# Optimization experiments

Measured on AMD Instinct MI355X. Metric: run time of the kernel, lower is better.

## Reference

```python
import jax, jax.numpy as jnp
import numpy as np

N_CONTEXT = 9
N_INPUT = 26
WINDOW = 2 * N_CONTEXT + 1  # 19
BATCH, TIME = 64, 2000


def setup_inputs() -> dict:
    key = jax.random.key(0)
    x = jax.random.normal(key, (BATCH, TIME, N_INPUT), dtype=jnp.float32)
    return {"x": x}


def reference(x):
    # The original uses conv1d with an identity filter of shape
    # (window, channels, window*channels) and SAME padding. That is exactly
    # a zero-padded sliding-window unfold: output[b, t] = flatten of
    # x[b, t-n_context : t+n_context+1, :] (zero padded at edges).
    B, T, C = x.shape
    xp = jnp.pad(x, ((0, 0), (N_CONTEXT, N_CONTEXT), (0, 0)))  # [B, T+2*ctx, C]
    # gather indices for each output position: [T, WINDOW]
    idx = jnp.arange(T)[:, None] + jnp.arange(WINDOW)[None, :]
    win = xp[:, idx, :]  # [B, T, WINDOW, C]
    return win.reshape(-1, WINDOW * C)  # [B*T, WINDOW*C]
```

## Files before the change

kernel.cpp:

```cpp
#include <hip/hip_runtime.h>

constexpr int N_CONTEXT = 9;
constexpr int C         = 26;
constexpr int WINDOW    = 2 * N_CONTEXT + 1;
constexpr int BATCH     = 64;
constexpr int TIME      = 2000;
constexpr int ROW       = WINDOW * C;

constexpr int T_TILE      = 16;
constexpr int LDS_ROWS    = T_TILE + WINDOW - 1;
constexpr int LDS_FLOATS  = LDS_ROWS * C;
constexpr int TILE_FLOATS = T_TILE * ROW;
constexpr int TILE_VEC4   = TILE_FLOATS / 4;
constexpr int BLOCK       = 256;
constexpr int NBLOCKS     = BATCH * TIME / T_TILE;
constexpr int BATCH_FLOATS = TIME * C;

typedef float vfloat4 __attribute__((ext_vector_type(4)));

__global__ __launch_bounds__(BLOCK)
void CreateOverlappingWindows_84963043050043_kernel(const float* __restrict__ x,
                                                    float* __restrict__ out) {
    __shared__ float lds[LDS_FLOATS];
    const int blk = blockIdx.x;
    const int tid = threadIdx.x;
    const int r0  = blk * T_TILE;
    const int b   = r0 / TIME;
    const int lo  = b * BATCH_FLOATS;
    const int g0  = (r0 - N_CONTEXT) * C;

    #pragma unroll
    for (int it = 0; it < (LDS_FLOATS + BLOCK - 1) / BLOCK; ++it) {
        int idx = tid + it * BLOCK;
        if (idx < LDS_FLOATS) {
            int g = g0 + idx;
            lds[idx] = ((unsigned)(g - lo) < (unsigned)BATCH_FLOATS) ? x[g] : 0.0f;
        }
    }
    __syncthreads();

    const float2* lds2 = reinterpret_cast<const float2*>(lds);
    vfloat4* out4 = reinterpret_cast<vfloat4*>(out) + (size_t)blk * TILE_VEC4;
    #pragma unroll
    for (int it = 0; it < (TILE_VEC4 + BLOCK - 1) / BLOCK; ++it) {
        int q = tid + it * BLOCK;
        if (q < TILE_VEC4) {
            int f  = q * 4;
            int lt = f / ROW;
            int j  = f - lt * ROW;
            int a  = lt * C + j;
            int sub = (j == ROW - 2) ? (ROW - C) : 0;
            float2 p0 = lds2[a >> 1];
            float2 p1 = lds2[(a + 2 - sub) >> 1];
            vfloat4 v; v.x = p0.x; v.y = p0.y; v.z = p1.x; v.w = p1.y;
            out4[q] = v;
        }
    }
}

extern "C" void kernel_launch(void* const* d_in, const int* in_sizes, int n_in,
                              void* d_out, int out_size, void* d_ws, size_t ws_size,
                              hipStream_t stream) {
    const float* x = (const float*)d_in[0];
    float* out = (float*)d_out;
    CreateOverlappingWindows_84963043050043_kernel<<<NBLOCKS, BLOCK, 0, stream>>>(x, out);
}
```

Measured before the change: 252.8 us.

## Enlarge time tile and write output as per-column float2 streams

Raises the tile from 16 to 40 timesteps so the halo overhead per block shrinks, and loads the input into LDS as float2. The output phase now gives each of 247 threads one float2 column and loops over the 40 rows, replacing the earlier flat float4 write with its per-element index math. In exchange, stores are 8-byte rather than 16-byte, 9 of 256 threads sit idle during writes, and a block has 40 dependent store iterations, which may lower memory-level parallelism on a write-bound kernel.

```diff
diff --git a/kernel.cpp b/kernel.cpp
--- a/kernel.cpp
+++ b/kernel.cpp
@@ -6,54 +6,45 @@
 constexpr int BATCH     = 64;
 constexpr int TIME      = 2000;
 constexpr int ROW       = WINDOW * C;
+constexpr int ROW2      = ROW / 2;
+constexpr int C2        = C / 2;
 
-constexpr int T_TILE      = 16;
-constexpr int LDS_ROWS    = T_TILE + WINDOW - 1;
-constexpr int LDS_FLOATS  = LDS_ROWS * C;
-constexpr int TILE_FLOATS = T_TILE * ROW;
-constexpr int TILE_VEC4   = TILE_FLOATS / 4;
-constexpr int BLOCK       = 256;
-constexpr int NBLOCKS     = BATCH * TIME / T_TILE;
-constexpr int BATCH_FLOATS = TIME * C;
-
-typedef float vfloat4 __attribute__((ext_vector_type(4)));
+constexpr int T_TILE    = 40;
+constexpr int LDS_ROWS  = T_TILE + WINDOW - 1;
+constexpr int LDS_F2    = LDS_ROWS * C2;
+constexpr int BLOCK     = 256;
+constexpr int NBLOCKS   = BATCH * TIME / T_TILE;
+constexpr int BATCH_F2  = TIME * C2;
 
 __global__ __launch_bounds__(BLOCK)
 void CreateOverlappingWindows_84963043050043_kernel(const float* __restrict__ x,
                                                     float* __restrict__ out) {
-    __shared__ float lds[LDS_FLOATS];
+    __shared__ float2 lds2[LDS_F2];
     const int blk = blockIdx.x;
     const int tid = threadIdx.x;
     const int r0  = blk * T_TILE;
     const int b   = r0 / TIME;
-    const int lo  = b * BATCH_FLOATS;
-    const int g0  = (r0 - N_CONTEXT) * C;
+    const int lo2 = b * BATCH_F2;
+    const int base2 = ((r0 - N_CONTEXT) * C) >> 1;
+    const float2* x2 = reinterpret_cast<const float2*>(x);
 
     #pragma unroll
-    for (int it = 0; it < (LDS_FLOATS + BLOCK - 1) / BLOCK; ++it) {
+    for (int it = 0; it < (LDS_F2 + BLOCK - 1) / BLOCK; ++it) {
         int idx = tid + it * BLOCK;
-        if (idx < LDS_FLOATS) {
-            int g = g0 + idx;
-            lds[idx] = ((unsigned)(g - lo) < (unsigned)BATCH_FLOATS) ? x[g] : 0.0f;
+        if (idx < LDS_F2) {
+            int g = base2 + idx;
+            float2 v = make_float2(0.0f, 0.0f);
+            if ((unsigned)(g - lo2) < (unsigned)BATCH_F2) v = x2[g];
+            lds2[idx] = v;
         }
     }
     __syncthreads();
 
-    const float2* lds2 = reinterpret_cast<const float2*>(lds);
-    vfloat4* out4 = reinterpret_cast<vfloat4*>(out) + (size_t)blk * TILE_VEC4;
-    #pragma unroll
-    for (int it = 0; it < (TILE_VEC4 + BLOCK - 1) / BLOCK; ++it) {
-        int q = tid + it * BLOCK;
-        if (q < TILE_VEC4) {
-            int f  = q * 4;
-            int lt = f / ROW;
-            int j  = f - lt * ROW;
-            int a  = lt * C + j;
-            int sub = (j == ROW - 2) ? (ROW - C) : 0;
-            float2 p0 = lds2[a >> 1];
-            float2 p1 = lds2[(a + 2 - sub) >> 1];
-            vfloat4 v; v.x = p0.x; v.y = p0.y; v.z = p1.x; v.w = p1.y;
-            out4[q] = v;
+    if (tid < ROW2) {
+        float2* o2 = reinterpret_cast<float2*>(out) + (size_t)r0 * ROW2 + tid;
+        #pragma unroll
+        for (int lt = 0; lt < T_TILE; ++lt) {
+            o2[(size_t)lt * ROW2] = lds2[lt * C2 + tid];
         }
     }
 }
```

After: 253.9 us. No clear change (+0.4%).
